# Performance work log

Measured on AMD Instinct MI355X. Metric: run time of the kernel, lower is better.

Reference implementation:

```python
import jax, jax.numpy as jnp
import numpy as np

N = 500000      # examples = M * (nr+1)
K = 20          # context set size (indices[:, 3:])
NR = 24         # negatives per positive
H = 128         # hidden_channels == node feature dim
NODES = 10000   # ingredient vocabulary


def setup_inputs() -> dict:
    key = jax.random.key(0)
    ks = jax.random.split(key, 6)
    indices = jax.random.randint(ks[0], (N, 3 + K), 0, NODES)
    x = jax.random.normal(ks[1], (NODES, H), dtype=jnp.float32)
    scale = 0.02
    W1 = jax.random.normal(ks[2], (H, 3 * H), dtype=jnp.float32) * scale
    b1 = jnp.zeros((H,), jnp.float32)
    W2 = jax.random.normal(ks[3], (H // 2, H), dtype=jnp.float32) * scale
    b2 = jnp.zeros((H // 2,), jnp.float32)
    W3 = jax.random.normal(ks[4], (1, H // 2), dtype=jnp.float32) * scale
    b3 = jnp.zeros((1,), jnp.float32)
    return {"indices": indices, "nr": NR, "x": x,
            "W1": W1, "b1": b1, "W2": W2, "b2": b2, "W3": W3, "b3": b3}


def _embed_context(ctx_idx, x, nr):
    # ctx_idx: [N, K]; one context row per group of (nr+1) examples
    new_idx = ctx_idx[:-1:nr + 1]                 # [M, K]
    emb = x[new_idx]                               # [M, K, H] gather
    s = emb.sum(axis=1)                            # [M, H]
    norm = jnp.maximum((new_idx > 0).sum(axis=1), 1).astype(x.dtype)[:, None]
    mean = s / norm                                # masked mean over context
    return jnp.repeat(mean, nr + 1, axis=0)        # broadcast back to [N, H]


def reference(indices, nr, x, W1, b1, W2, b2, W3, b3):
    ing1 = x[indices[:, 0]]                        # [N, H]
    ing2 = x[indices[:, 1]]                        # [N, H]
    set_emb = _embed_context(indices[:, 3:], x, nr)  # [N, H]
    y = jnp.concatenate([ing1, ing2, set_emb], axis=1)  # [N, 3H]
    y = jax.nn.relu(y @ W1.T + b1)
    y = jax.nn.relu(y @ W2.T + b2)
    return y @ W3.T + b3                           # [N, 1]
```

## Files before the change

### kernel.cpp

```cpp
#include <hip/hip_runtime.h>
#include <hip/hip_bf16.h>

#define N_ROWS   500000
#define NR1      25
#define NGROUPS  20000
#define KCTX     20
#define H        128
#define NODES    10000
#define IDX_COLS 23

typedef __attribute__((ext_vector_type(8))) short short8;
typedef __attribute__((ext_vector_type(4))) float f32x4;

__device__ __forceinline__ unsigned pkbf(float lo, float hi) {
  __hip_bfloat162 h = __float22bfloat162_rn(make_float2(lo, hi));
  union { __hip_bfloat162 h; unsigned u; } c; c.h = h;
  return c.u;
}
__device__ __forceinline__ float lo2f(unsigned u) {
  union { unsigned u; float f; } c; c.u = u << 16; return c.f;
}
__device__ __forceinline__ float hi2f(unsigned u) {
  union { unsigned u; float f; } c; c.u = u & 0xffff0000u; return c.f;
}

#define GPB 8
#define MEAN_BLOCKS (NGROUPS / GPB)
__global__ __launch_bounds__(256) void k_means(
    const int* __restrict__ indices, const float* __restrict__ x,
    unsigned short* __restrict__ gm) {
  const int tid = threadIdx.x;
  const int sub = tid >> 6;
  const int jj  = (tid & 63) * 2;
#pragma unroll
  for (int it = 0; it < GPB / 4; ++it) {
    const int g = blockIdx.x * GPB + it * 4 + sub;
    const int* __restrict__ rowidx =
        indices + (size_t)g * NR1 * IDX_COLS + 3;
    float s0 = 0.f, s1 = 0.f;
    int cnt = 0;
#pragma unroll
    for (int c = 0; c < KCTX; ++c) {
      const int idx = rowidx[c];
      const float2 v = *(const float2*)(x + (size_t)idx * H + jj);
      s0 += v.x; s1 += v.y;
      cnt += (idx > 0) ? 1 : 0;
    }
    const float rn = 1.f / (float)((cnt > 1) ? cnt : 1);
    *(unsigned*)(gm + (size_t)g * H + jj) = pkbf(s0 * rn, s1 * rn);
  }
}

#define PN 64
#define PBLK  ((NODES + PN - 1) / PN)
#define GBLK  ((NGROUPS + PN - 1) / PN)
#define B_PG  (4 * PBLK)
#define B_W2F (B_PG + 2 * GBLK)
#define PRE_BLOCKS (B_W2F + 1)

__global__ __launch_bounds__(256) void k_precompute(
    const float* __restrict__ x, const float* __restrict__ W1,
    const float* __restrict__ b1, const unsigned short* __restrict__ gm,
    const float* __restrict__ W2,
    unsigned short* __restrict__ Pb, float* __restrict__ Pg,
    unsigned short* __restrict__ w2f) {
  const int tid = threadIdx.x;
  const int bid = blockIdx.x;

  const int lane = tid & 63;
  const int wvid = tid >> 6;
  const int col  = lane & 15;
  const int quad = lane >> 4;

  if (bid == B_W2F) {
#pragma unroll
    for (int i = 0; i < 4; ++i) {
      const int fi = i * 4 + wvid;
      const int kt = fi >> 2, ct = fi & 3;
      const float* __restrict__ src =
          W2 + (size_t)(ct * 16 + col) * H + kt * 32 + quad * 8;
      const float4 v0 = *(const float4*)src;
      const float4 v1 = *(const float4*)(src + 4);
      union { short8 v; unsigned u[4]; } pk;
      pk.u[0] = pkbf(v0.x, v0.y);
      pk.u[1] = pkbf(v0.z, v0.w);
      pk.u[2] = pkbf(v1.x, v1.y);
      pk.u[3] = pkbf(v1.z, v1.w);
      *(short8*)(w2f + (size_t)(fi * 64 + lane) * 8) = pk.v;
    }
    return;
  }

  __shared__ __align__(16) short wlds[64 * 128];

  const bool isPg = (bid >= B_PG);
  int m, sub;
  if (isPg) { m = 2; sub = bid - B_PG; }
  else      { m = bid / (2 * PBLK); sub = bid - m * (2 * PBLK); }
  const int tbase = (sub >> 1) * PN;
  const int ch    = sub & 1;

#pragma unroll
  for (int it = 0; it < 8; ++it) {
    const int f  = it * 256 + tid;
    const int j  = f >> 5;
    const int q4 = f & 31;
    const float4 v =
        *(const float4*)(W1 + (size_t)(ch * 64 + j) * (3 * H) + m * H + q4 * 4);
    const int sidx = j * 128 + (((q4 >> 1) ^ (j & 7)) << 3) + (q4 & 1) * 4;
    *(unsigned*)&wlds[sidx]     = pkbf(v.x, v.y);
    *(unsigned*)&wlds[sidx + 2] = pkbf(v.z, v.w);
  }
  __syncthreads();

  short8 Af[4];
  if (isPg) {
    int g = tbase + wvid * 16 + col;
    if (g > NGROUPS - 1) g = NGROUPS - 1;
    const short8* __restrict__ gr = (const short8*)(gm + (size_t)g * H);
#pragma unroll
    for (int kt = 0; kt < 4; ++kt) Af[kt] = gr[kt * 4 + quad];
  } else {
    int node = tbase + wvid * 16 + col;
    if (node > NODES - 1) node = NODES - 1;
    const float4* __restrict__ xr = (const float4*)(x + (size_t)node * H);
#pragma unroll
    for (int kt = 0; kt < 4; ++kt) {
      const int f4 = kt * 8 + quad * 2;
      const float4 v0 = xr[f4], v1 = xr[f4 + 1];
      union { short8 v; unsigned u[4]; } pk;
      pk.u[0] = pkbf(v0.x, v0.y);
      pk.u[1] = pkbf(v0.z, v0.w);
      pk.u[2] = pkbf(v1.x, v1.y);
      pk.u[3] = pkbf(v1.z, v1.w);
      Af[kt] = pk.v;
    }
  }

  f32x4 acc[4];
#pragma unroll
  for (int ct = 0; ct < 4; ++ct) acc[ct] = (f32x4)(0.f);

#pragma unroll
  for (int kt = 0; kt < 4; ++kt) {
#pragma unroll
    for (int ct = 0; ct < 4; ++ct) {
      const int brow = ct * 16 + col;
      const short8 Bf = *(const short8*)
          &wlds[brow * 128 + (((kt * 4 + quad) ^ (brow & 7)) << 3)];
      acc[ct] = __builtin_amdgcn_mfma_f32_16x16x32_bf16(Af[kt], Bf, acc[ct], 0, 0, 0);
    }
  }

  if (isPg) {
    float b1v[4];
#pragma unroll
    for (int ct = 0; ct < 4; ++ct) b1v[ct] = b1[ch * 64 + ct * 16 + col];
#pragma unroll
    for (int reg = 0; reg < 4; ++reg) {
      const int g = tbase + wvid * 16 + quad * 4 + reg;
      if (g < NGROUPS) {
#pragma unroll
        for (int ct = 0; ct < 4; ++ct)
          Pg[(size_t)g * H + ch * 64 + ct * 16 + col] = acc[ct][reg] + b1v[ct];
      }
    }
  } else {
    unsigned short* __restrict__ Pm = Pb + (size_t)m * NODES * H;
#pragma unroll
    for (int reg = 0; reg < 4; ++reg) {
      const int n = tbase + wvid * 16 + quad * 4 + reg;
      if (n < NODES) {
#pragma unroll
        for (int ct = 0; ct < 4; ++ct) {
          union { unsigned u; unsigned short s[2]; } c;
          c.u = pkbf(acc[ct][reg], 0.f);
          Pm[(size_t)n * H + ch * 64 + ct * 16 + col] = c.s[0];
        }
      }
    }
  }
}

__global__ __launch_bounds__(256, 4) void k_main(
    const int* __restrict__ indices,
    const unsigned short* __restrict__ P1b, const unsigned short* __restrict__ P2b,
    const float* __restrict__ Pg, const unsigned short* __restrict__ w2f,
    const float* __restrict__ b2, const float* __restrict__ W3,
    const float* __restrict__ b3, float* __restrict__ out) {
  const int tid  = threadIdx.x;
  const int lane = tid & 63;
  const int wv   = tid >> 6;
  const int col  = lane & 15;
  const int quad = lane >> 4;

  const int Rw = (blockIdx.x * 4 + wv) * 16;
  const int r  = Rw + col;
  const int rc = (r < N_ROWS) ? r : (N_ROWS - 1);

  const int i0 = indices[(size_t)rc * IDX_COLS + 0];
  const int i1 = indices[(size_t)rc * IDX_COLS + 1];
  const int g  = rc / NR1;

  const short8* __restrict__ pa = (const short8*)(P1b + (size_t)i0 * H);
  const short8* __restrict__ pb = (const short8*)(P2b + (size_t)i1 * H);
  short8 ua[4], ub[4];
#pragma unroll
  for (int kt = 0; kt < 4; ++kt) {
    ua[kt] = pa[kt * 4 + quad];
    ub[kt] = pb[kt * 4 + quad];
  }

  const float* __restrict__ cg = Pg + (size_t)g * H;
  float4 c0[4], c1[4];
#pragma unroll
  for (int kt = 0; kt < 4; ++kt) {
    c0[kt] = *(const float4*)(cg + kt * 32 + quad * 8);
    c1[kt] = *(const float4*)(cg + kt * 32 + quad * 8 + 4);
  }

  float b2v[4], w3v[4];
#pragma unroll
  for (int ct = 0; ct < 4; ++ct) {
    b2v[ct] = b2[ct * 16 + col];
    w3v[ct] = W3[ct * 16 + col];
  }
  const float bias3 = b3[0];

  short8 A[4];
#pragma unroll
  for (int kt = 0; kt < 4; ++kt) {
    union { short8 v; unsigned u[4]; } va, vb;
    va.v = ua[kt]; vb.v = ub[kt];
    const float h0 = fmaxf(lo2f(va.u[0]) + lo2f(vb.u[0]) + c0[kt].x, 0.f);
    const float h1 = fmaxf(hi2f(va.u[0]) + hi2f(vb.u[0]) + c0[kt].y, 0.f);
    const float h2 = fmaxf(lo2f(va.u[1]) + lo2f(vb.u[1]) + c0[kt].z, 0.f);
    const float h3 = fmaxf(hi2f(va.u[1]) + hi2f(vb.u[1]) + c0[kt].w, 0.f);
    const float h4 = fmaxf(lo2f(va.u[2]) + lo2f(vb.u[2]) + c1[kt].x, 0.f);
    const float h5 = fmaxf(hi2f(va.u[2]) + hi2f(vb.u[2]) + c1[kt].y, 0.f);
    const float h6 = fmaxf(lo2f(va.u[3]) + lo2f(vb.u[3]) + c1[kt].z, 0.f);
    const float h7 = fmaxf(hi2f(va.u[3]) + hi2f(vb.u[3]) + c1[kt].w, 0.f);
    union { short8 v; unsigned u[4]; } pk;
    pk.u[0] = pkbf(h0, h1);
    pk.u[1] = pkbf(h2, h3);
    pk.u[2] = pkbf(h4, h5);
    pk.u[3] = pkbf(h6, h7);
    A[kt] = pk.v;
  }

  f32x4 acc[4];
#pragma unroll
  for (int ct = 0; ct < 4; ++ct) acc[ct] = (f32x4)(0.f);
#pragma unroll
  for (int kt = 0; kt < 4; ++kt) {
#pragma unroll
    for (int ct = 0; ct < 4; ++ct) {
      const short8 Bf =
          *(const short8*)(w2f + (size_t)((kt * 4 + ct) * 64 + lane) * 8);
      acc[ct] = __builtin_amdgcn_mfma_f32_16x16x32_bf16(A[kt], Bf, acc[ct], 0, 0, 0);
    }
  }

#pragma unroll
  for (int reg = 0; reg < 4; ++reg) {
    float s = 0.f;
#pragma unroll
    for (int ct = 0; ct < 4; ++ct)
      s += fmaxf(acc[ct][reg] + b2v[ct], 0.f) * w3v[ct];
    s += __shfl_xor(s, 1);
    s += __shfl_xor(s, 2);
    s += __shfl_xor(s, 4);
    s += __shfl_xor(s, 8);
    if (col == 0) {
      const int row = Rw + quad * 4 + reg;
      if (row < N_ROWS) out[row] = s + bias3;
    }
  }
}

extern "C" void kernel_launch(void* const* d_in, const int* in_sizes, int n_in,
                              void* d_out, int out_size, void* d_ws, size_t ws_size,
                              hipStream_t stream) {
  const int*   indices = (const int*)  d_in[0];
  const float* x  = (const float*)d_in[2];
  const float* W1 = (const float*)d_in[3];
  const float* b1 = (const float*)d_in[4];
  const float* W2 = (const float*)d_in[5];
  const float* b2 = (const float*)d_in[6];
  const float* W3 = (const float*)d_in[7];
  const float* b3 = (const float*)d_in[8];
  float* out = (float*)d_out;

  unsigned short* Pb  = (unsigned short*)d_ws;
  unsigned short* P1b = Pb;
  unsigned short* P2b = Pb + (size_t)NODES * H;
  unsigned short* gm  = Pb + (size_t)2 * NODES * H;
  float* Pg = (float*)(gm + (size_t)NGROUPS * H);
  unsigned short* w2f = (unsigned short*)(Pg + (size_t)NGROUPS * H);

  k_means<<<MEAN_BLOCKS, 256, 0, stream>>>(indices, x, gm);
  k_precompute<<<PRE_BLOCKS, 256, 0, stream>>>(x, W1, b1, gm, W2, Pb, Pg, w2f);
  k_main<<<(N_ROWS + 63) / 64, 256, 0, stream>>>(indices, P1b, P2b, Pg, w2f,
                                                 b2, W3, b3, out);
}
```

Before: 169.9 us.

## Project context nodes through W1 before averaging; process two row tiles per wave

The mean-then-project order for the context embedding is reversed. Every node is projected by the third W1 slice (P3b) in the precompute kernel, and k_ctx then averages the bf16 projected rows per group and adds b1. This removes the separate means kernel and the group GEMM. The context term is now stored as bf16 instead of fp32, so k_main loads less data. k_main also handles 32 rows per wave and stages W2 fragments in shared memory once per block, so each B fragment is reused across two MFMAs. The costs are slightly more bf16 rounding and a heavier register load per wave.

```diff
diff --git a/kernel.cpp b/kernel.cpp
--- a/kernel.cpp
+++ b/kernel.cpp
@@ -24,46 +24,15 @@
   union { unsigned u; float f; } c; c.u = u & 0xffff0000u; return c.f;
 }
 
-#define GPB 8
-#define MEAN_BLOCKS (NGROUPS / GPB)
-__global__ __launch_bounds__(256) void k_means(
-    const int* __restrict__ indices, const float* __restrict__ x,
-    unsigned short* __restrict__ gm) {
-  const int tid = threadIdx.x;
-  const int sub = tid >> 6;
-  const int jj  = (tid & 63) * 2;
-#pragma unroll
-  for (int it = 0; it < GPB / 4; ++it) {
-    const int g = blockIdx.x * GPB + it * 4 + sub;
-    const int* __restrict__ rowidx =
-        indices + (size_t)g * NR1 * IDX_COLS + 3;
-    float s0 = 0.f, s1 = 0.f;
-    int cnt = 0;
-#pragma unroll
-    for (int c = 0; c < KCTX; ++c) {
-      const int idx = rowidx[c];
-      const float2 v = *(const float2*)(x + (size_t)idx * H + jj);
-      s0 += v.x; s1 += v.y;
-      cnt += (idx > 0) ? 1 : 0;
-    }
-    const float rn = 1.f / (float)((cnt > 1) ? cnt : 1);
-    *(unsigned*)(gm + (size_t)g * H + jj) = pkbf(s0 * rn, s1 * rn);
-  }
-}
-
 #define PN 64
 #define PBLK  ((NODES + PN - 1) / PN)
-#define GBLK  ((NGROUPS + PN - 1) / PN)
-#define B_PG  (4 * PBLK)
-#define B_W2F (B_PG + 2 * GBLK)
+#define B_W2F (6 * PBLK)
 #define PRE_BLOCKS (B_W2F + 1)
 
 __global__ __launch_bounds__(256) void k_precompute(
     const float* __restrict__ x, const float* __restrict__ W1,
-    const float* __restrict__ b1, const unsigned short* __restrict__ gm,
     const float* __restrict__ W2,
-    unsigned short* __restrict__ Pb, float* __restrict__ Pg,
-    unsigned short* __restrict__ w2f) {
+    unsigned short* __restrict__ Pb, unsigned short* __restrict__ w2f) {
   const int tid = threadIdx.x;
   const int bid = blockIdx.x;
 
@@ -93,10 +62,9 @@
 
   __shared__ __align__(16) short wlds[64 * 128];
 
-  const bool isPg = (bid >= B_PG);
-  int m, sub;
-  if (isPg) { m = 2; sub = bid - B_PG; }
-  else      { m = bid / (2 * PBLK); sub = bid - m * (2 * PBLK); }
+  const int m   = bid / (2 * PBLK);
+  const int sub = bid - m * (2 * PBLK);
+  const int mcol = (m == 2) ? 2 : m;
   const int tbase = (sub >> 1) * PN;
   const int ch    = sub & 1;
 
@@ -106,35 +74,27 @@
     const int j  = f >> 5;
     const int q4 = f & 31;
     const float4 v =
-        *(const float4*)(W1 + (size_t)(ch * 64 + j) * (3 * H) + m * H + q4 * 4);
+        *(const float4*)(W1 + (size_t)(ch * 64 + j) * (3 * H) + mcol * H + q4 * 4);
     const int sidx = j * 128 + (((q4 >> 1) ^ (j & 7)) << 3) + (q4 & 1) * 4;
     *(unsigned*)&wlds[sidx]     = pkbf(v.x, v.y);
     *(unsigned*)&wlds[sidx + 2] = pkbf(v.z, v.w);
   }
   __syncthreads();
 
+  int node = tbase + wvid * 16 + col;
+  if (node > NODES - 1) node = NODES - 1;
+  const float4* __restrict__ xr = (const float4*)(x + (size_t)node * H);
   short8 Af[4];
-  if (isPg) {
-    int g = tbase + wvid * 16 + col;
-    if (g > NGROUPS - 1) g = NGROUPS - 1;
-    const short8* __restrict__ gr = (const short8*)(gm + (size_t)g * H);
-#pragma unroll
-    for (int kt = 0; kt < 4; ++kt) Af[kt] = gr[kt * 4 + quad];
-  } else {
-    int node = tbase + wvid * 16 + col;
-    if (node > NODES - 1) node = NODES - 1;
-    const float4* __restrict__ xr = (const float4*)(x + (size_t)node * H);
-#pragma unroll
-    for (int kt = 0; kt < 4; ++kt) {
-      const int f4 = kt * 8 + quad * 2;
-      const float4 v0 = xr[f4], v1 = xr[f4 + 1];
-      union { short8 v; unsigned u[4]; } pk;
-      pk.u[0] = pkbf(v0.x, v0.y);
-      pk.u[1] = pkbf(v0.z, v0.w);
-      pk.u[2] = pkbf(v1.x, v1.y);
-      pk.u[3] = pkbf(v1.z, v1.w);
-      Af[kt] = pk.v;
-    }
+#pragma unroll
+  for (int kt = 0; kt < 4; ++kt) {
+    const int f4 = kt * 8 + quad * 2;
+    const float4 v0 = xr[f4], v1 = xr[f4 + 1];
+    union { short8 v; unsigned u[4]; } pk;
+    pk.u[0] = pkbf(v0.x, v0.y);
+    pk.u[1] = pkbf(v0.z, v0.w);
+    pk.u[2] = pkbf(v1.x, v1.y);
+    pk.u[3] = pkbf(v1.z, v1.w);
+    Af[kt] = pk.v;
   }
 
   f32x4 acc[4];
@@ -152,72 +112,104 @@
     }
   }
 
-  if (isPg) {
-    float b1v[4];
-#pragma unroll
-    for (int ct = 0; ct < 4; ++ct) b1v[ct] = b1[ch * 64 + ct * 16 + col];
-#pragma unroll
-    for (int reg = 0; reg < 4; ++reg) {
-      const int g = tbase + wvid * 16 + quad * 4 + reg;
-      if (g < NGROUPS) {
-#pragma unroll
-        for (int ct = 0; ct < 4; ++ct)
-          Pg[(size_t)g * H + ch * 64 + ct * 16 + col] = acc[ct][reg] + b1v[ct];
+  unsigned short* __restrict__ Pm = Pb + (size_t)m * NODES * H;
+#pragma unroll
+  for (int reg = 0; reg < 4; ++reg) {
+    const int n = tbase + wvid * 16 + quad * 4 + reg;
+    if (n < NODES) {
+#pragma unroll
+      for (int ct = 0; ct < 4; ++ct) {
+        union { unsigned u; unsigned short s[2]; } c;
+        c.u = pkbf(acc[ct][reg], 0.f);
+        Pm[(size_t)n * H + ch * 64 + ct * 16 + col] = c.s[0];
       }
     }
-  } else {
-    unsigned short* __restrict__ Pm = Pb + (size_t)m * NODES * H;
-#pragma unroll
-    for (int reg = 0; reg < 4; ++reg) {
-      const int n = tbase + wvid * 16 + quad * 4 + reg;
-      if (n < NODES) {
-#pragma unroll
-        for (int ct = 0; ct < 4; ++ct) {
-          union { unsigned u; unsigned short s[2]; } c;
-          c.u = pkbf(acc[ct][reg], 0.f);
-          Pm[(size_t)n * H + ch * 64 + ct * 16 + col] = c.s[0];
-        }
-      }
-    }
-  }
-}
-
+  }
+}
+
+#define GPB 8
+#define CTX_BLOCKS (NGROUPS / GPB)
+__global__ __launch_bounds__(256) void k_ctx(
+    const int* __restrict__ indices, const unsigned short* __restrict__ P3b,
+    const float* __restrict__ b1, unsigned short* __restrict__ Pgb) {
+  const int tid  = threadIdx.x;
+  const int sub  = tid >> 6;
+  const int lane = tid & 63;
+  const int jj   = lane * 2;
+  const float2 b1v = *(const float2*)(b1 + jj);
+#pragma unroll
+  for (int it = 0; it < GPB / 4; ++it) {
+    const int g = blockIdx.x * GPB + it * 4 + sub;
+    const int* __restrict__ rowidx =
+        indices + (size_t)g * NR1 * IDX_COLS + 3;
+    float s0 = 0.f, s1 = 0.f;
+    int cnt = 0;
+#pragma unroll
+    for (int c = 0; c < KCTX; ++c) {
+      const int idx = rowidx[c];
+      const unsigned w = *(const unsigned*)(P3b + (size_t)idx * H + jj);
+      s0 += lo2f(w); s1 += hi2f(w);
+      cnt += (idx > 0) ? 1 : 0;
+    }
+    const float rn = 1.f / (float)((cnt > 1) ? cnt : 1);
+    *(unsigned*)(Pgb + (size_t)g * H + jj) = pkbf(b1v.x + s0 * rn, b1v.y + s1 * rn);
+  }
+}
+
+#define RPW 32
 __global__ __launch_bounds__(256, 4) void k_main(
     const int* __restrict__ indices,
     const unsigned short* __restrict__ P1b, const unsigned short* __restrict__ P2b,
-    const float* __restrict__ Pg, const unsigned short* __restrict__ w2f,
+    const unsigned short* __restrict__ Pgb, const unsigned short* __restrict__ w2f,
     const float* __restrict__ b2, const float* __restrict__ W3,
     const float* __restrict__ b3, float* __restrict__ out) {
+  __shared__ __align__(16) short w2s[16 * 64 * 8];
+
   const int tid  = threadIdx.x;
   const int lane = tid & 63;
   const int wv   = tid >> 6;
   const int col  = lane & 15;
   const int quad = lane >> 4;
 
-  const int Rw = (blockIdx.x * 4 + wv) * 16;
-  const int r  = Rw + col;
-  const int rc = (r < N_ROWS) ? r : (N_ROWS - 1);
-
-  const int i0 = indices[(size_t)rc * IDX_COLS + 0];
-  const int i1 = indices[(size_t)rc * IDX_COLS + 1];
-  const int g  = rc / NR1;
-
-  const short8* __restrict__ pa = (const short8*)(P1b + (size_t)i0 * H);
-  const short8* __restrict__ pb = (const short8*)(P2b + (size_t)i1 * H);
-  short8 ua[4], ub[4];
-#pragma unroll
-  for (int kt = 0; kt < 4; ++kt) {
-    ua[kt] = pa[kt * 4 + quad];
-    ub[kt] = pb[kt * 4 + quad];
-  }
-
-  const float* __restrict__ cg = Pg + (size_t)g * H;
-  float4 c0[4], c1[4];
-#pragma unroll
-  for (int kt = 0; kt < 4; ++kt) {
-    c0[kt] = *(const float4*)(cg + kt * 32 + quad * 8);
-    c1[kt] = *(const float4*)(cg + kt * 32 + quad * 8 + 4);
-  }
+  {
+    const short8* __restrict__ src = (const short8*)w2f;
+    short8* dst = (short8*)w2s;
+#pragma unroll
+    for (int i = 0; i < 4; ++i) dst[i * 256 + tid] = src[i * 256 + tid];
+  }
+  __syncthreads();
+
+  const int Rw = (blockIdx.x * 4 + wv) * RPW;
+  const int r0 = Rw + col, r1 = Rw + 16 + col;
+  const int rc0 = (r0 < N_ROWS) ? r0 : (N_ROWS - 1);
+  const int rc1 = (r1 < N_ROWS) ? r1 : (N_ROWS - 1);
+  const int g0 = rc0 / NR1, g1 = rc1 / NR1;
+
+  const short8* __restrict__ pc0 = (const short8*)(Pgb + (size_t)g0 * H);
+  const short8* __restrict__ pc1 = (const short8*)(Pgb + (size_t)g1 * H);
+  short8 uc0[4], uc1[4];
+#pragma unroll
+  for (int kt = 0; kt < 4; ++kt) {
+    uc0[kt] = pc0[kt * 4 + quad];
+    uc1[kt] = pc1[kt * 4 + quad];
+  }
+
+  const int2 iA = *(const int2*)(indices + (size_t)rc0 * IDX_COLS);
+  const int2 iB = *(const int2*)(indices + (size_t)rc1 * IDX_COLS);
+
+  const short8* __restrict__ pa0 = (const short8*)(P1b + (size_t)iA.x * H);
+  const short8* __restrict__ pb0 = (const short8*)(P2b + (size_t)iA.y * H);
+  const short8* __restrict__ pa1 = (const short8*)(P1b + (size_t)iB.x * H);
+  const short8* __restrict__ pb1 = (const short8*)(P2b + (size_t)iB.y * H);
+  short8 ua0[4], ub0[4], ua1[4], ub1[4];
+#pragma unroll
+  for (int kt = 0; kt < 4; ++kt) {
+    ua0[kt] = pa0[kt * 4 + quad];
+    ub0[kt] = pb0[kt * 4 + quad];
+    ua1[kt] = pa1[kt * 4 + quad];
+    ub1[kt] = pb1[kt * 4 + quad];
+  }
+  __builtin_amdgcn_sched_barrier(0);
 
   float b2v[4], w3v[4];
 #pragma unroll
@@ -227,53 +219,65 @@
   }
   const float bias3 = b3[0];
 
-  short8 A[4];
-#pragma unroll
-  for (int kt = 0; kt < 4; ++kt) {
-    union { short8 v; unsigned u[4]; } va, vb;
-    va.v = ua[kt]; vb.v = ub[kt];
-    const float h0 = fmaxf(lo2f(va.u[0]) + lo2f(vb.u[0]) + c0[kt].x, 0.f);
-    const float h1 = fmaxf(hi2f(va.u[0]) + hi2f(vb.u[0]) + c0[kt].y, 0.f);
-    const float h2 = fmaxf(lo2f(va.u[1]) + lo2f(vb.u[1]) + c0[kt].z, 0.f);
-    const float h3 = fmaxf(hi2f(va.u[1]) + hi2f(vb.u[1]) + c0[kt].w, 0.f);
-    const float h4 = fmaxf(lo2f(va.u[2]) + lo2f(vb.u[2]) + c1[kt].x, 0.f);
-    const float h5 = fmaxf(hi2f(va.u[2]) + hi2f(vb.u[2]) + c1[kt].y, 0.f);
-    const float h6 = fmaxf(lo2f(va.u[3]) + lo2f(vb.u[3]) + c1[kt].z, 0.f);
-    const float h7 = fmaxf(hi2f(va.u[3]) + hi2f(vb.u[3]) + c1[kt].w, 0.f);
+  short8 A0[4], A1[4];
+#pragma unroll
+  for (int kt = 0; kt < 4; ++kt) {
+    union { short8 v; unsigned u[4]; } va, vb, vc;
+    va.v = ua0[kt]; vb.v = ub0[kt]; vc.v = uc0[kt];
     union { short8 v; unsigned u[4]; } pk;
-    pk.u[0] = pkbf(h0, h1);
-    pk.u[1] = pkbf(h2, h3);
-    pk.u[2] = pkbf(h4, h5);
-    pk.u[3] = pkbf(h6, h7);
-    A[kt] = pk.v;
-  }
-
-  f32x4 acc[4];
-#pragma unroll
-  for (int ct = 0; ct < 4; ++ct) acc[ct] = (f32x4)(0.f);
+#pragma unroll
+    for (int w = 0; w < 4; ++w) {
+      const float hl = fmaxf(lo2f(va.u[w]) + lo2f(vb.u[w]) + lo2f(vc.u[w]), 0.f);
+      const float hh = fmaxf(hi2f(va.u[w]) + hi2f(vb.u[w]) + hi2f(vc.u[w]), 0.f);
+      pk.u[w] = pkbf(hl, hh);
+    }
+    A0[kt] = pk.v;
+  }
+#pragma unroll
+  for (int kt = 0; kt < 4; ++kt) {
+    union { short8 v; unsigned u[4]; } va, vb, vc;
+    va.v = ua1[kt]; vb.v = ub1[kt]; vc.v = uc1[kt];
+    union { short8 v; unsigned u[4]; } pk;
+#pragma unroll
+    for (int w = 0; w < 4; ++w) {
+      const float hl = fmaxf(lo2f(va.u[w]) + lo2f(vb.u[w]) + lo2f(vc.u[w]), 0.f);
+      const float hh = fmaxf(hi2f(va.u[w]) + hi2f(vb.u[w]) + hi2f(vc.u[w]), 0.f);
+      pk.u[w] = pkbf(hl, hh);
+    }
+    A1[kt] = pk.v;
+  }
+
+  f32x4 acc0[4], acc1[4];
+#pragma unroll
+  for (int ct = 0; ct < 4; ++ct) { acc0[ct] = (f32x4)(0.f); acc1[ct] = (f32x4)(0.f); }
 #pragma unroll
   for (int kt = 0; kt < 4; ++kt) {
 #pragma unroll
     for (int ct = 0; ct < 4; ++ct) {
-      const short8 Bf =
-          *(const short8*)(w2f + (size_t)((kt * 4 + ct) * 64 + lane) * 8);
-      acc[ct] = __builtin_amdgcn_mfma_f32_16x16x32_bf16(A[kt], Bf, acc[ct], 0, 0, 0);
-    }
-  }
-
-#pragma unroll
-  for (int reg = 0; reg < 4; ++reg) {
-    float s = 0.f;
-#pragma unroll
-    for (int ct = 0; ct < 4; ++ct)
-      s += fmaxf(acc[ct][reg] + b2v[ct], 0.f) * w3v[ct];
-    s += __shfl_xor(s, 1);
-    s += __shfl_xor(s, 2);
-    s += __shfl_xor(s, 4);
-    s += __shfl_xor(s, 8);
-    if (col == 0) {
-      const int row = Rw + quad * 4 + reg;
-      if (row < N_ROWS) out[row] = s + bias3;
+      const short8 Bf = *(const short8*)&w2s[((kt * 4 + ct) * 64 + lane) * 8];
+      acc0[ct] = __builtin_amdgcn_mfma_f32_16x16x32_bf16(A0[kt], Bf, acc0[ct], 0, 0, 0);
+      acc1[ct] = __builtin_amdgcn_mfma_f32_16x16x32_bf16(A1[kt], Bf, acc1[ct], 0, 0, 0);
+    }
+  }
+
+#pragma unroll
+  for (int grp = 0; grp < 2; ++grp) {
+#pragma unroll
+    for (int reg = 0; reg < 4; ++reg) {
+      float s = 0.f;
+#pragma unroll
+      for (int ct = 0; ct < 4; ++ct) {
+        const float a = (grp == 0) ? acc0[ct][reg] : acc1[ct][reg];
+        s += fmaxf(a + b2v[ct], 0.f) * w3v[ct];
+      }
+      s += __shfl_xor(s, 1);
+      s += __shfl_xor(s, 2);
+      s += __shfl_xor(s, 4);
+      s += __shfl_xor(s, 8);
+      if (col == 0) {
+        const int row = Rw + grp * 16 + quad * 4 + reg;
+        if (row < N_ROWS) out[row] = s + bias3;
+      }
     }
   }
 }
@@ -294,12 +298,12 @@
   unsigned short* Pb  = (unsigned short*)d_ws;
   unsigned short* P1b = Pb;
   unsigned short* P2b = Pb + (size_t)NODES * H;
-  unsigned short* gm  = Pb + (size_t)2 * NODES * H;
-  float* Pg = (float*)(gm + (size_t)NGROUPS * H);
-  unsigned short* w2f = (unsigned short*)(Pg + (size_t)NGROUPS * H);
-
-  k_means<<<MEAN_BLOCKS, 256, 0, stream>>>(indices, x, gm);
-  k_precompute<<<PRE_BLOCKS, 256, 0, stream>>>(x, W1, b1, gm, W2, Pb, Pg, w2f);
-  k_main<<<(N_ROWS + 63) / 64, 256, 0, stream>>>(indices, P1b, P2b, Pg, w2f,
-                                                 b2, W3, b3, out);
-}
+  unsigned short* P3b = Pb + (size_t)2 * NODES * H;
+  unsigned short* Pgb = Pb + (size_t)3 * NODES * H;
+  unsigned short* w2f = Pgb + (size_t)NGROUPS * H;
+
+  k_precompute<<<PRE_BLOCKS, 256, 0, stream>>>(x, W1, W2, Pb, w2f);
+  k_ctx<<<CTX_BLOCKS, 256, 0, stream>>>(indices, P3b, b1, Pgb);
+  k_main<<<(N_ROWS + 4 * RPW - 1) / (4 * RPW), 256, 0, stream>>>(
+      indices, P1b, P2b, Pgb, w2f, b2, W3, b3, out);
+}
```

New measurement: 149.8 us. 1.13x faster.
